# Kernel tuning notes

Measured on AMD Instinct MI355X. Metric: run time of the kernel, lower is better.

Reference implementation:

```python
import jax, jax.numpy as jnp
import numpy as np

C, H2, E, SQ, SK, HW = 256, 256, 512, 2048, 64, 256

def setup_inputs() -> dict:
    key = jax.random.key(0)
    ks = jax.random.split(key, 12)
    s = 0.05
    return {
        "Z": jax.random.normal(ks[0], (C, HW, HW), jnp.float32),
        "Q": jax.random.normal(ks[1], (SQ, 3), jnp.float32),
        "q_z": jax.random.normal(ks[2], (SQ, C), jnp.float32),
        "r": jax.random.uniform(ks[3], (SQ, SK, 2), jnp.float32) * (HW - 2),
        "w1": jax.random.normal(ks[4], (H2, 2), jnp.float32) * s,
        "b1": jnp.zeros((H2,), jnp.float32),
        "w2": jax.random.normal(ks[5], (H2, 3), jnp.float32) * s,
        "b2": jnp.zeros((H2,), jnp.float32),
        "in_proj_w": jax.random.normal(ks[6], (3 * E, E), jnp.float32) * s,
        "in_proj_b": jnp.zeros((3 * E,), jnp.float32),
        "out_proj_w": jax.random.normal(ks[7], (E, E), jnp.float32) * s,
        "out_proj_b": jnp.zeros((E,), jnp.float32),
        "num_heads": 8,
    }

def bilinear_interpolation_3d(Z, x, y):
    # Z: [c, H, W]; x, y: [N] float coords. Faithful to torch: .int() trunc (coords >= 0)
    c = Z.shape[0]
    x1 = x.astype(jnp.int32)
    y1 = y.astype(jnp.int32)
    x2 = x1 + 1
    y2 = y1 + 1
    Q11 = Z[:, x1, y1]  # [c, N]
    Q12 = Z[:, x1, y2]
    Q21 = Z[:, x2, y1]
    Q22 = Z[:, x2, y2]
    dx = x - x1
    dy = y - y1
    R1 = Q11 * (1 - dx) + Q21 * dx
    R2 = Q12 * (1 - dx) + Q22 * dx
    interp = R1 * (1 - dy) + R2 * dy  # [c, N]
    # faithful to the original: raw row-major reshape (NOT a transpose)
    return jnp.reshape(interp, (-1, c))

def reference(Z, Q, q_z, r, w1, b1, w2, b2, in_proj_w, in_proj_b, out_proj_w, out_proj_b, num_heads):
    size_q, size_k, _ = r.shape
    qr = r.reshape(-1, 2)
    Zr = bilinear_interpolation_3d(Z, qr[:, 0], qr[:, 1])
    Zr = Zr.reshape(size_q, size_k, -1)  # [sq, sk, c]
    r_proj = r @ w1.T + b1               # [sq, sk, h2]
    key = jnp.concatenate([Zr, r_proj], axis=2)  # [sq, sk, E]
    value = key
    q_proj = Q @ w2.T + b2               # [sq, h2]
    query = jnp.concatenate([q_z, q_proj], axis=1)  # [sq, E]
    E_ = query.shape[1]
    hd = E_ // num_heads
    # torch MultiheadAttention in-projection
    ql = query @ in_proj_w[:E_].T + in_proj_b[:E_]              # [sq, E]
    kl = key @ in_proj_w[E_:2 * E_].T + in_proj_b[E_:2 * E_]    # [sq, sk, E]
    vl = value @ in_proj_w[2 * E_:].T + in_proj_b[2 * E_:]
    qh = ql.reshape(size_q, num_heads, hd)
    kh = kl.reshape(size_q, size_k, num_heads, hd)
    vh = vl.reshape(size_q, size_k, num_heads, hd)
    scores = jnp.einsum('bhd,bkhd->bhk', qh, kh) / jnp.sqrt(jnp.asarray(hd, qh.dtype))
    attn = jax.nn.softmax(scores, axis=-1)  # [sq, h, sk]
    out = jnp.einsum('bhk,bkhd->bhd', attn, vh).reshape(size_q, E_)
    out = out @ out_proj_w.T + out_proj_b
    return jnp.concatenate([q_z, out], axis=1)  # [sq, c + E]
```

## Files before the change

### kernel.cpp

```cpp
#include <hip/hip_runtime.h>


typedef _Float16 half8 __attribute__((ext_vector_type(8)));
typedef _Float16 half4v __attribute__((ext_vector_type(4)));
typedef float f32x4 __attribute__((ext_vector_type(4)));

#define O_QRY   1048576u
#define O_WCT   2097152u
#define O_MT    4194304u
#define O_U     6291456u
#define O_G     14680064u
#define O_ZT    23068672u
#define O_ZR    39845888u
#define O_F32   73400320u

__global__ __launch_bounds__(256) void k_pre(
    const float* __restrict__ Z, const float* __restrict__ ipw,
    const float* __restrict__ opw, const float* __restrict__ q_z,
    const float* __restrict__ Qm, const float* __restrict__ w2,
    const float* __restrict__ b2, const float* __restrict__ ipb,
    const float* __restrict__ opb,
    _Float16* __restrict__ wsh, float* __restrict__ bu, float* __restrict__ b_eff)
{
    __shared__ __align__(16) unsigned char sbuf[33792];
    int b = blockIdx.x, t = threadIdx.x;

    if (b < 2048) {
        float (*sT)[33] = (float(*)[33])sbuf;
        int x = b >> 3, yt = (b & 7) * 32;
#pragma unroll
        for (int i = 0; i < 8; ++i) {
            int g = i * 256 + t;
            int c = g >> 3, y = (g & 7) * 4;
            float4 v = *(const float4*)(Z + (size_t)c * 65536 + x * 256 + yt + y);
            sT[c][y] = v.x; sT[c][y + 1] = v.y; sT[c][y + 2] = v.z; sT[c][y + 3] = v.w;
        }
        __syncthreads();
        _Float16* Zt = wsh + O_ZT;
        int c4 = (t & 63) * 4;
#pragma unroll
        for (int i = 0; i < 8; ++i) {
            int y = (t >> 6) * 8 + i;
            half4v o;
#pragma unroll
            for (int j = 0; j < 4; ++j) o[j] = (_Float16)sT[c4 + j][y];
            *(half4v*)(Zt + ((size_t)(x * 256 + yt + y)) * 256 + c4) = o;
        }
    } else if (b < 3072) {
        int e4 = ((b - 2048) * 256 + t) * 4;
        int q = e4 >> 9, j = e4 & 511;
        half4v o;
        if (j < 256) {
            float4 v = *(const float4*)(q_z + q * 256 + j);
            o[0] = (_Float16)v.x; o[1] = (_Float16)v.y;
            o[2] = (_Float16)v.z; o[3] = (_Float16)v.w;
        } else {
            float q0 = Qm[q * 3], q1 = Qm[q * 3 + 1], q2 = Qm[q * 3 + 2];
#pragma unroll
            for (int u = 0; u < 4; ++u) {
                int m = j - 256 + u;
                o[u] = (_Float16)(q0 * w2[m * 3] + q1 * w2[m * 3 + 1] + q2 * w2[m * 3 + 2] + b2[m]);
            }
        }
        *(half4v*)(wsh + O_QRY + e4) = o;
    } else if (b < 4096) {
        int isMt = (b >= 3584);
        int b2 = b - (isMt ? 3584 : 3072);
        int h = b2 >> 6, jt = (b2 >> 3) & 7, lt = b2 & 7;
        _Float16 (*sAm)[72] = (_Float16(*)[72])sbuf;
        _Float16 (*sBn)[72] = (_Float16(*)[72])(sbuf + 9216);
        int j0 = jt * 64, l0 = lt * 64;
        int dd = t >> 4, c4 = (t & 15) * 4;
#pragma unroll
        for (int ii = 0; ii < 4; ++ii) {
            int d = ii * 16 + dd;
            if (!isMt) {
                float4 k4 = *(const float4*)(ipw + (size_t)(512 + h * 64 + d) * 512 + j0 + c4);
                float4 q4 = *(const float4*)(ipw + (size_t)(h * 64 + d) * 512 + l0 + c4);
                sAm[c4 + 0][d] = (_Float16)(0.125f * k4.x);
                sAm[c4 + 1][d] = (_Float16)(0.125f * k4.y);
                sAm[c4 + 2][d] = (_Float16)(0.125f * k4.z);
                sAm[c4 + 3][d] = (_Float16)(0.125f * k4.w);
                sBn[c4 + 0][d] = (_Float16)q4.x;
                sBn[c4 + 1][d] = (_Float16)q4.y;
                sBn[c4 + 2][d] = (_Float16)q4.z;
                sBn[c4 + 3][d] = (_Float16)q4.w;
            } else {
                int e = ii * 16 + dd;
                float4 o4 = *(const float4*)(opw + (size_t)(l0 + e) * 512 + h * 64 + c4);
                half4v ov;
                ov[0] = (_Float16)o4.x; ov[1] = (_Float16)o4.y;
                ov[2] = (_Float16)o4.z; ov[3] = (_Float16)o4.w;
                *(half4v*)&sAm[e][c4] = ov;
                float4 v4 = *(const float4*)(ipw + (size_t)(1024 + h * 64 + d) * 512 + j0 + c4);
                sBn[c4 + 0][d] = (_Float16)v4.x;
                sBn[c4 + 1][d] = (_Float16)v4.y;
                sBn[c4 + 2][d] = (_Float16)v4.z;
                sBn[c4 + 3][d] = (_Float16)v4.w;
            }
        }
        __syncthreads();
        int w = t >> 6, l = t & 63;
        int arow = l & 15, kg = (l >> 4) << 3;
        f32x4 acc[4] = {};
#pragma unroll
        for (int kk = 0; kk < 64; kk += 32) {
            half8 a = *(const half8*)&sAm[w * 16 + arow][kk + kg];
#pragma unroll
            for (int nt = 0; nt < 4; ++nt) {
                half8 bb = *(const half8*)&sBn[nt * 16 + arow][kk + kg];
                acc[nt] = __builtin_amdgcn_mfma_f32_16x16x32_f16(a, bb, acc[nt], 0, 0, 0);
            }
        }
        int rg = (l >> 4) << 2;
        if (!isMt) {
            _Float16* Wc = wsh + O_WCT;
#pragma unroll
            for (int nt = 0; nt < 4; ++nt)
#pragma unroll
                for (int v = 0; v < 4; ++v)
                    Wc[(size_t)(h * 512 + j0 + w * 16 + rg + v) * 512 + l0 + nt * 16 + arow] =
                        (_Float16)acc[nt][v];
        } else {
            _Float16* Mt = wsh + O_MT;
#pragma unroll
            for (int nt = 0; nt < 4; ++nt)
#pragma unroll
                for (int v = 0; v < 4; ++v)
                    Mt[(size_t)(l0 + w * 16 + rg + v) * 4096 + h * 512 + j0 + nt * 16 + arow] =
                        (_Float16)acc[nt][v];
        }
    } else if (b < 4112) {
        int c = (b - 4096) * 256 + t;
        int h = c >> 9, j = c & 511;
        float s = 0.f;
#pragma unroll 4
        for (int d = 0; d < 64; ++d)
            s += ipb[512 + (h << 6) + d] * ipw[(size_t)(512 + (h << 6) + d) * 512 + j];
        bu[c] = 0.125f * s;
    } else {
        int e = (b - 4112) * 4 + (t >> 6), l = t & 63;
        const float* worow = opw + (size_t)e * 512;
        float s = 0.f;
#pragma unroll
        for (int i = 0; i < 8; ++i)
            s += ipb[1024 + l + 64 * i] * worow[l + 64 * i];
#pragma unroll
        for (int mm = 1; mm < 64; mm <<= 1) s += __shfl_xor(s, mm, 64);
        if (l == 0) b_eff[e] = s + opb[e];
    }
}

__global__ __launch_bounds__(256, 6) void k_mid(
    const float* __restrict__ r, _Float16* __restrict__ wsh,
    const float* __restrict__ bu)
{
    __shared__ __align__(16) unsigned char smem[16896];
    int b = blockIdx.x, t = threadIdx.x, w = t >> 6, l = t & 63;

    if (b < 1024) {
        _Float16 (*sA)[136] = (_Float16(*)[136])smem;
        const _Float16* A = wsh + O_QRY;
        const _Float16* B = wsh + O_WCT;
        _Float16* U = wsh + O_U;
        int q0 = (b & 63) * 32;
        int colb = (b >> 6) * 256 + w * 64;
        f32x4 acc[2][4] = {};
        int arow = l & 15, kg = (l >> 4) << 3;
#pragma unroll
        for (int s = 0; s < 4; ++s) {
#pragma unroll
            for (int i = 0; i < 2; ++i) {
                int e = i * 2048 + t * 8;
                *(half8*)&sA[e >> 7][e & 127] =
                    *(const half8*)(A + (size_t)(q0 + (e >> 7)) * 512 + s * 128 + (e & 127));
            }
            __syncthreads();
#pragma unroll
            for (int kk = 0; kk < 128; kk += 32) {
                half8 a[2], bb[4];
#pragma unroll
                for (int mt = 0; mt < 2; ++mt) a[mt] = *(const half8*)&sA[mt * 16 + arow][kk + kg];
#pragma unroll
                for (int nt = 0; nt < 4; ++nt)
                    bb[nt] = *(const half8*)(B + (size_t)(colb + nt * 16 + arow) * 512 + s * 128 + kk + kg);
#pragma unroll
                for (int mt = 0; mt < 2; ++mt)
#pragma unroll
                    for (int nt = 0; nt < 4; ++nt)
                        acc[mt][nt] = __builtin_amdgcn_mfma_f32_16x16x32_f16(a[mt], bb[nt], acc[mt][nt], 0, 0, 0);
            }
            __syncthreads();
        }
#pragma unroll
        for (int mt = 0; mt < 2; ++mt)
#pragma unroll
            for (int nt = 0; nt < 4; ++nt)
#pragma unroll
                for (int v = 0; v < 4; ++v) {
                    int row = q0 + mt * 16 + ((l >> 4) << 2) + v;
                    int col = colb + nt * 16 + arow;
                    U[(size_t)row * 4096 + col] = (_Float16)(acc[mt][nt][v] + bu[col]);
                }
    } else {
        _Float16 (*sT)[264] = (_Float16(*)[264])smem;
        const _Float16* Zt = wsh + O_ZT;
        _Float16* Zr = wsh + O_ZR;
        int pb = b - 1024;
        const float2* r2 = (const float2*)r;
        int hb = l >> 5, ch0 = (l & 31) * 8;
#pragma unroll
        for (int i = 0; i < 4; ++i) {
            int ptl = i * 8 + w * 2 + hb;
            float2 rv = r2[pb * 32 + ptl];
            int x1 = (int)rv.x, y1 = (int)rv.y;
            float dx = rv.x - (float)x1, dy = rv.y - (float)y1;
            float w11 = (1.f - dx) * (1.f - dy), w21 = dx * (1.f - dy);
            float w12 = (1.f - dx) * dy,         w22 = dx * dy;
            const _Float16* base = Zt + ((size_t)(x1 * 256 + y1)) * 256 + ch0;
            half8 z11 = *(const half8*)(base);
            half8 z12 = *(const half8*)(base + 256);
            half8 z21 = *(const half8*)(base + 65536);
            half8 z22 = *(const half8*)(base + 65536 + 256);
            half8 o;
#pragma unroll
            for (int c = 0; c < 8; ++c)
                o[c] = (_Float16)(w11 * (float)z11[c] + w21 * (float)z21[c]
                                + w12 * (float)z12[c] + w22 * (float)z22[c]);
            *(half8*)&sT[ptl][ch0] = o;
        }
        __syncthreads();
        int ch_ = t >> 2, pt8 = (t & 3) * 8;
#pragma unroll
        for (int g = 0; g < 4; ++g) {
            int ch = g * 64 + ch_;
            half8 o;
#pragma unroll
            for (int j = 0; j < 8; ++j) o[j] = sT[pt8 + j][ch];
            *(half8*)(Zr + (size_t)ch * 131072 + pb * 32 + pt8) = o;
        }
    }
}

__global__ __launch_bounds__(512, 2) void k_main(
    const _Float16* __restrict__ Zr, const float* __restrict__ r,
    const float* __restrict__ w1, const float* __restrict__ b1,
    const _Float16* __restrict__ U, _Float16* __restrict__ G)
{
    __shared__ __align__(16) _Float16 sKey[64][520];
    __shared__ __align__(16) _Float16 sU[8][520];
    __shared__ float sP[512];
    __shared__ float sP2[512];
    __shared__ __align__(16) _Float16 sA16[16][72];

    int q = blockIdx.x;
    int t = threadIdx.x, w = t >> 6, l = t & 63;
    int ch = q >> 3, s8 = q & 7;

    for (int i = t; i < 576; i += 512) ((unsigned*)sA16)[i] = 0u;

    const _Float16* src = Zr + ((size_t)ch * 2048 + s8 * 256) * 64;
#pragma unroll
    for (int i = 0; i < 4; ++i) {
        int e = i * 4096 + t * 8;
        *(half8*)&sKey[e >> 8][e & 255] = *(const half8*)(src + e);
    }
    {
        int e = t * 8;
        *(half8*)&sU[e >> 9][e & 511] = *(const half8*)(U + (size_t)q * 4096 + e);
    }
    {
        int m = t & 255, half = t >> 8;
        float w10 = w1[2 * m], w11 = w1[2 * m + 1], b1m = b1[m];
        const float2* r2q = (const float2*)r + (size_t)q * 64;
#pragma unroll 8
        for (int i = 0; i < 32; ++i) {
            int k = half * 32 + i;
            float2 rv = r2q[k];
            sKey[k][256 + m] = (_Float16)(rv.x * w10 + rv.y * w11 + b1m);
        }
    }
    __syncthreads();

    {
        f32x4 acc = {};
        int arow = l & 15, kg = (l >> 4) << 3;
        int wm = w & 3, khalf = (w >> 2) << 8;
        const _Float16* ar = &sKey[wm * 16 + arow][khalf + kg];
        const _Float16* br = &sU[l & 7][khalf + kg];
#pragma unroll
        for (int kk = 0; kk < 256; kk += 32)
            acc = __builtin_amdgcn_mfma_f32_16x16x32_f16(
                *(const half8*)(ar + kk), *(const half8*)(br + kk), acc, 0, 0, 0);
        if ((l & 15) < 8) {
            int h = l & 15, krow0 = wm * 16 + ((l >> 4) << 2);
            float* dst = (w < 4) ? sP : sP2;
#pragma unroll
            for (int v = 0; v < 4; ++v) dst[(h << 6) + krow0 + v] = acc[v];
        }
    }
    __syncthreads();

    {
        float v = sP[t] + sP2[t];
        float mx = v;
#pragma unroll
        for (int mm = 1; mm < 64; mm <<= 1) mx = fmaxf(mx, __shfl_xor(mx, mm, 64));
        float e = __expf(v - mx);
        float sm = e;
#pragma unroll
        for (int mm = 1; mm < 64; mm <<= 1) sm += __shfl_xor(sm, mm, 64);
        sA16[w][l] = (_Float16)(e / sm);
    }
    __syncthreads();

    {
        f32x4 acc[4] = {};
        int arow = l & 15, kq = (l >> 4) << 3;
        half8 a0 = *(const half8*)&sA16[arow][kq];
        half8 a1 = *(const half8*)&sA16[arow][32 + kq];
#pragma unroll
        for (int nt = 0; nt < 4; ++nt) {
            int n0 = (w << 6) + (nt << 4);
            half8 b0, b1f;
#pragma unroll
            for (int jj = 0; jj < 8; ++jj) b0[jj] = sKey[kq + jj][n0 + arow];
            acc[nt] = __builtin_amdgcn_mfma_f32_16x16x32_f16(a0, b0, acc[nt], 0, 0, 0);
#pragma unroll
            for (int jj = 0; jj < 8; ++jj) b1f[jj] = sKey[32 + kq + jj][n0 + arow];
            acc[nt] = __builtin_amdgcn_mfma_f32_16x16x32_f16(a1, b1f, acc[nt], 0, 0, 0);
        }
        if (l < 32) {
            int rgrp = (l >> 4) << 2;
#pragma unroll
            for (int nt = 0; nt < 4; ++nt) {
                int n0 = (w << 6) + (nt << 4);
#pragma unroll
                for (int v = 0; v < 4; ++v)
                    sU[rgrp + v][n0 + arow] = (_Float16)acc[nt][v];
            }
        }
    }
    __syncthreads();

    {
        int c = t * 8;
        *(half8*)(G + (size_t)q * 4096 + c) = *(const half8*)&sU[c >> 9][c & 511];
    }
}

__global__ __launch_bounds__(256) void k_final(
    const _Float16* __restrict__ G, const _Float16* __restrict__ Mt,
    const float* __restrict__ b_eff, const float* __restrict__ qz,
    float* __restrict__ out)
{
    __shared__ __align__(16) _Float16 sA[32][520];
    int rb = blockIdx.x, cb = blockIdx.y;
    int q0 = rb * 32;
    int t = threadIdx.x, w = t >> 6, l = t & 63;

    if (cb == 0) {
#pragma unroll
        for (int i = 0; i < 8; ++i) {
            int idx4 = i * 256 + t;
            int row = idx4 >> 6, c = (idx4 & 63) << 2;
            *(float4*)&out[(size_t)(q0 + row) * 768 + c] =
                *(const float4*)&qz[(size_t)(q0 + row) * 256 + c];
        }
    }

    f32x4 acc[2][2] = {};
    int arow = l & 15, kg = (l >> 4) << 3;
    int e0 = cb * 128 + (w << 5);
    for (int c = 0; c < 8; ++c) {
#pragma unroll
        for (int i = 0; i < 8; ++i) {
            int e = i * 2048 + t * 8;
            *(half8*)&sA[e >> 9][e & 511] =
                *(const half8*)(G + (size_t)(q0 + (e >> 9)) * 4096 + c * 512 + (e & 511));
        }
        __syncthreads();
#pragma unroll 4
        for (int kk = 0; kk < 512; kk += 32) {
            half8 a[2], bb[2];
#pragma unroll
            for (int nt = 0; nt < 2; ++nt)
                bb[nt] = *(const half8*)(Mt + (size_t)(e0 + nt * 16 + arow) * 4096 + c * 512 + kk + kg);
#pragma unroll
            for (int mt = 0; mt < 2; ++mt) {
                a[mt] = *(const half8*)&sA[mt * 16 + arow][kk + kg];
#pragma unroll
                for (int nt = 0; nt < 2; ++nt)
                    acc[mt][nt] = __builtin_amdgcn_mfma_f32_16x16x32_f16(a[mt], bb[nt], acc[mt][nt], 0, 0, 0);
            }
        }
        __syncthreads();
    }
#pragma unroll
    for (int mt = 0; mt < 2; ++mt)
#pragma unroll
        for (int nt = 0; nt < 2; ++nt)
#pragma unroll
            for (int v = 0; v < 4; ++v) {
                int row = q0 + mt * 16 + ((l >> 4) << 2) + v;
                int ecol = e0 + nt * 16 + arow;
                out[(size_t)row * 768 + 256 + ecol] = acc[mt][nt][v] + b_eff[ecol];
            }
}

extern "C" void kernel_launch(void* const* d_in, const int* in_sizes, int n_in,
                              void* d_out, int out_size, void* d_ws, size_t ws_size,
                              hipStream_t stream) {
    const float* Z          = (const float*)d_in[0];
    const float* Qm         = (const float*)d_in[1];
    const float* q_z        = (const float*)d_in[2];
    const float* r          = (const float*)d_in[3];
    const float* w1         = (const float*)d_in[4];
    const float* b1         = (const float*)d_in[5];
    const float* w2         = (const float*)d_in[6];
    const float* b2         = (const float*)d_in[7];
    const float* in_proj_w  = (const float*)d_in[8];
    const float* in_proj_b  = (const float*)d_in[9];
    const float* out_proj_w = (const float*)d_in[10];
    const float* out_proj_b = (const float*)d_in[11];
    float* out = (float*)d_out;

    _Float16* wsh = (_Float16*)d_ws;
    _Float16* Mt    = wsh + O_MT;
    _Float16* U     = wsh + O_U;
    _Float16* G     = wsh + O_G;
    _Float16* Zr    = wsh + O_ZR;
    float*    bu    = (float*)(wsh + O_F32);
    float*    b_eff = bu + 4096;

    k_pre<<<4240, 256, 0, stream>>>(Z, in_proj_w, out_proj_w, q_z, Qm, w2, b2,
                                    in_proj_b, out_proj_b, wsh, bu, b_eff);
    k_mid<<<5120, 256, 0, stream>>>(r, wsh, bu);
    k_main<<<2048, 512, 0, stream>>>(Zr, r, w1, b1, U, G);
    k_final<<<dim3(64, 4), 256, 0, stream>>>(G, Mt, b_eff, q_z, out);
}
```

Measured before the change: 288.6 us.

## Enlarge k_mid GEMM tiles, rework gather transpose, swizzle k_main shared key

The k_mid GEMM now computes 64x256 tiles per block with K staged in two 256-wide halves, which halves the block count and doubles reuse of the B operand loaded from global memory. The bilinear gather is restructured so each wave handles whole points with coalesced half2 channel loads into a padded fp32 transpose buffer. In k_main, the shared key tile uses an XOR column swizzle on both its writes and its reads to reduce LDS bank conflicts in the strided column reads for the attention-times-value MFMA. In exchange, k_mid uses twice the shared memory, more accumulator registers and a lower occupancy hint of 4.

Measured after the change: 271.9 us. 1.06x faster.

```diff
diff --git a/kernel.cpp b/kernel.cpp
--- a/kernel.cpp
+++ b/kernel.cpp
@@ -3,6 +3,7 @@
 
 typedef _Float16 half8 __attribute__((ext_vector_type(8)));
 typedef _Float16 half4v __attribute__((ext_vector_type(4)));
+typedef _Float16 half2v __attribute__((ext_vector_type(2)));
 typedef float f32x4 __attribute__((ext_vector_type(4)));
 
 #define O_QRY   1048576u
@@ -65,8 +66,8 @@
         *(half4v*)(wsh + O_QRY + e4) = o;
     } else if (b < 4096) {
         int isMt = (b >= 3584);
-        int b2 = b - (isMt ? 3584 : 3072);
-        int h = b2 >> 6, jt = (b2 >> 3) & 7, lt = b2 & 7;
+        int b2_ = b - (isMt ? 3584 : 3072);
+        int h = b2_ >> 6, jt = (b2_ >> 3) & 7, lt = b2_ & 7;
         _Float16 (*sAm)[72] = (_Float16(*)[72])sbuf;
         _Float16 (*sBn)[72] = (_Float16(*)[72])(sbuf + 9216);
         int j0 = jt * 64, l0 = lt * 64;
@@ -151,41 +152,41 @@
     }
 }
 
-__global__ __launch_bounds__(256, 6) void k_mid(
+__global__ __launch_bounds__(256, 4) void k_mid(
     const float* __restrict__ r, _Float16* __restrict__ wsh,
     const float* __restrict__ bu)
 {
-    __shared__ __align__(16) unsigned char smem[16896];
+    __shared__ __align__(16) unsigned char smem[33792];
     int b = blockIdx.x, t = threadIdx.x, w = t >> 6, l = t & 63;
 
-    if (b < 1024) {
-        _Float16 (*sA)[136] = (_Float16(*)[136])smem;
+    if (b < 512) {
+        _Float16 (*sA)[264] = (_Float16(*)[264])smem;
         const _Float16* A = wsh + O_QRY;
         const _Float16* B = wsh + O_WCT;
         _Float16* U = wsh + O_U;
-        int q0 = (b & 63) * 32;
-        int colb = (b >> 6) * 256 + w * 64;
-        f32x4 acc[2][4] = {};
+        int q0 = (b & 31) * 64;
+        int colb = (b >> 5) * 256 + w * 64;
+        f32x4 acc[4][4] = {};
         int arow = l & 15, kg = (l >> 4) << 3;
 #pragma unroll
-        for (int s = 0; s < 4; ++s) {
-#pragma unroll
-            for (int i = 0; i < 2; ++i) {
+        for (int half = 0; half < 2; ++half) {
+#pragma unroll
+            for (int i = 0; i < 8; ++i) {
                 int e = i * 2048 + t * 8;
-                *(half8*)&sA[e >> 7][e & 127] =
-                    *(const half8*)(A + (size_t)(q0 + (e >> 7)) * 512 + s * 128 + (e & 127));
+                *(half8*)&sA[e >> 8][e & 255] =
+                    *(const half8*)(A + (size_t)(q0 + (e >> 8)) * 512 + half * 256 + (e & 255));
             }
             __syncthreads();
-#pragma unroll
-            for (int kk = 0; kk < 128; kk += 32) {
-                half8 a[2], bb[4];
-#pragma unroll
-                for (int mt = 0; mt < 2; ++mt) a[mt] = *(const half8*)&sA[mt * 16 + arow][kk + kg];
+#pragma unroll 2
+            for (int kk = 0; kk < 256; kk += 32) {
+                half8 a[4], bb[4];
+#pragma unroll
+                for (int mt = 0; mt < 4; ++mt) a[mt] = *(const half8*)&sA[mt * 16 + arow][kk + kg];
 #pragma unroll
                 for (int nt = 0; nt < 4; ++nt)
-                    bb[nt] = *(const half8*)(B + (size_t)(colb + nt * 16 + arow) * 512 + s * 128 + kk + kg);
-#pragma unroll
-                for (int mt = 0; mt < 2; ++mt)
+                    bb[nt] = *(const half8*)(B + (size_t)(colb + nt * 16 + arow) * 512 + half * 256 + kk + kg);
+#pragma unroll
+                for (int mt = 0; mt < 4; ++mt)
 #pragma unroll
                     for (int nt = 0; nt < 4; ++nt)
                         acc[mt][nt] = __builtin_amdgcn_mfma_f32_16x16x32_f16(a[mt], bb[nt], acc[mt][nt], 0, 0, 0);
@@ -193,7 +194,7 @@
             __syncthreads();
         }
 #pragma unroll
-        for (int mt = 0; mt < 2; ++mt)
+        for (int mt = 0; mt < 4; ++mt)
 #pragma unroll
             for (int nt = 0; nt < 4; ++nt)
 #pragma unroll
@@ -203,41 +204,42 @@
                     U[(size_t)row * 4096 + col] = (_Float16)(acc[mt][nt][v] + bu[col]);
                 }
     } else {
-        _Float16 (*sT)[264] = (_Float16(*)[264])smem;
+        float (*sT)[33] = (float(*)[33])smem;
         const _Float16* Zt = wsh + O_ZT;
         _Float16* Zr = wsh + O_ZR;
-        int pb = b - 1024;
+        int pb = b - 512;
         const float2* r2 = (const float2*)r;
-        int hb = l >> 5, ch0 = (l & 31) * 8;
-#pragma unroll
-        for (int i = 0; i < 4; ++i) {
-            int ptl = i * 8 + w * 2 + hb;
+#pragma unroll 2
+        for (int i = 0; i < 8; ++i) {
+            int ptl = w * 8 + i;
             float2 rv = r2[pb * 32 + ptl];
             int x1 = (int)rv.x, y1 = (int)rv.y;
             float dx = rv.x - (float)x1, dy = rv.y - (float)y1;
             float w11 = (1.f - dx) * (1.f - dy), w21 = dx * (1.f - dy);
             float w12 = (1.f - dx) * dy,         w22 = dx * dy;
-            const _Float16* base = Zt + ((size_t)(x1 * 256 + y1)) * 256 + ch0;
-            half8 z11 = *(const half8*)(base);
-            half8 z12 = *(const half8*)(base + 256);
-            half8 z21 = *(const half8*)(base + 65536);
-            half8 z22 = *(const half8*)(base + 65536 + 256);
+            const _Float16* base = Zt + ((size_t)(x1 * 256 + y1)) * 256;
+#pragma unroll
+            for (int cg = 0; cg < 2; ++cg) {
+                int c = cg * 128 + l * 2;
+                half2v z11 = *(const half2v*)(base + c);
+                half2v z12 = *(const half2v*)(base + 256 + c);
+                half2v z21 = *(const half2v*)(base + 65536 + c);
+                half2v z22 = *(const half2v*)(base + 65536 + 256 + c);
+                sT[c][ptl]     = w11 * (float)z11[0] + w21 * (float)z21[0]
+                               + w12 * (float)z12[0] + w22 * (float)z22[0];
+                sT[c + 1][ptl] = w11 * (float)z11[1] + w21 * (float)z21[1]
+                               + w12 * (float)z12[1] + w22 * (float)z22[1];
+            }
+        }
+        __syncthreads();
+        int ch0 = t >> 2, colc = (t & 3) * 8;
+#pragma unroll
+        for (int g = 0; g < 4; ++g) {
+            int ch = g * 64 + ch0;
             half8 o;
 #pragma unroll
-            for (int c = 0; c < 8; ++c)
-                o[c] = (_Float16)(w11 * (float)z11[c] + w21 * (float)z21[c]
-                                + w12 * (float)z12[c] + w22 * (float)z22[c]);
-            *(half8*)&sT[ptl][ch0] = o;
-        }
-        __syncthreads();
-        int ch_ = t >> 2, pt8 = (t & 3) * 8;
-#pragma unroll
-        for (int g = 0; g < 4; ++g) {
-            int ch = g * 64 + ch_;
-            half8 o;
-#pragma unroll
-            for (int j = 0; j < 8; ++j) o[j] = sT[pt8 + j][ch];
-            *(half8*)(Zr + (size_t)ch * 131072 + pb * 32 + pt8) = o;
+            for (int j = 0; j < 8; ++j) o[j] = (_Float16)sT[ch][colc + j];
+            *(half8*)(Zr + (size_t)ch * 131072 + pb * 32 + colc) = o;
         }
     }
 }
@@ -263,7 +265,9 @@
 #pragma unroll
     for (int i = 0; i < 4; ++i) {
         int e = i * 4096 + t * 8;
-        *(half8*)&sKey[e >> 8][e & 255] = *(const half8*)(src + e);
+        int k = e >> 8, col = e & 255;
+        int colS = (((col >> 3) ^ (k >> 3)) << 3);
+        *(half8*)&sKey[k][colS] = *(const half8*)(src + e);
     }
     {
         int e = t * 8;
@@ -277,7 +281,9 @@
         for (int i = 0; i < 32; ++i) {
             int k = half * 32 + i;
             float2 rv = r2q[k];
-            sKey[k][256 + m] = (_Float16)(rv.x * w10 + rv.y * w11 + b1m);
+            int col = 256 + m;
+            int colS = ((((col >> 3) ^ (k >> 3)) << 3)) + (col & 7);
+            sKey[k][colS] = (_Float16)(rv.x * w10 + rv.y * w11 + b1m);
         }
     }
     __syncthreads();
@@ -286,12 +292,17 @@
         f32x4 acc = {};
         int arow = l & 15, kg = (l >> 4) << 3;
         int wm = w & 3, khalf = (w >> 2) << 8;
-        const _Float16* ar = &sKey[wm * 16 + arow][khalf + kg];
+        int k = wm * 16 + arow;
+        int sw = (k >> 3) & 7;
+        const _Float16* krow = &sKey[k][0];
         const _Float16* br = &sU[l & 7][khalf + kg];
 #pragma unroll
-        for (int kk = 0; kk < 256; kk += 32)
+        for (int kk = 0; kk < 256; kk += 32) {
+            int col = khalf + kk + kg;
+            half8 av = *(const half8*)(krow + ((((col >> 3) ^ sw) << 3)));
             acc = __builtin_amdgcn_mfma_f32_16x16x32_f16(
-                *(const half8*)(ar + kk), *(const half8*)(br + kk), acc, 0, 0, 0);
+                av, *(const half8*)(br + kk), acc, 0, 0, 0);
+        }
         if ((l & 15) < 8) {
             int h = l & 15, krow0 = wm * 16 + ((l >> 4) << 2);
             float* dst = (w < 4) ? sP : sP2;
@@ -317,17 +328,22 @@
     {
         f32x4 acc[4] = {};
         int arow = l & 15, kq = (l >> 4) << 3;
+        int sw0 = kq >> 3, sw1 = 4 + (kq >> 3);
         half8 a0 = *(const half8*)&sA16[arow][kq];
         half8 a1 = *(const half8*)&sA16[arow][32 + kq];
 #pragma unroll
         for (int nt = 0; nt < 4; ++nt) {
             int n0 = (w << 6) + (nt << 4);
+            int colb_ = n0 + arow;
+            int cg = colb_ >> 3, co = colb_ & 7;
+            int c0 = ((cg ^ sw0) << 3) + co;
+            int c1 = ((cg ^ sw1) << 3) + co;
             half8 b0, b1f;
 #pragma unroll
-            for (int jj = 0; jj < 8; ++jj) b0[jj] = sKey[kq + jj][n0 + arow];
+            for (int jj = 0; jj < 8; ++jj) b0[jj] = sKey[kq + jj][c0];
             acc[nt] = __builtin_amdgcn_mfma_f32_16x16x32_f16(a0, b0, acc[nt], 0, 0, 0);
 #pragma unroll
-            for (int jj = 0; jj < 8; ++jj) b1f[jj] = sKey[32 + kq + jj][n0 + arow];
+            for (int jj = 0; jj < 8; ++jj) b1f[jj] = sKey[32 + kq + jj][c1];
             acc[nt] = __builtin_amdgcn_mfma_f32_16x16x32_f16(a1, b1f, acc[nt], 0, 0, 0);
         }
         if (l < 32) {
@@ -435,7 +451,7 @@
 
     k_pre<<<4240, 256, 0, stream>>>(Z, in_proj_w, out_proj_w, q_z, Qm, w2, b2,
                                     in_proj_b, out_proj_b, wsh, bu, b_eff);
-    k_mid<<<5120, 256, 0, stream>>>(r, wsh, bu);
+    k_mid<<<4608, 256, 0, stream>>>(r, wsh, bu);
     k_main<<<2048, 512, 0, stream>>>(Zr, r, w1, b1, U, G);
     k_final<<<dim3(64, 4), 256, 0, stream>>>(G, Mt, b_eff, q_z, out);
 }
```
